# Kernel optimization log

Hardware: AMD Instinct MI355X
Metric: run time of the kernel (lower is better)

The kernel has to match this reference:

```python
import jax, jax.numpy as jnp
import numpy as np
import math

EPS = 1e-6  # PCEN eps


def _logit(p):
    return math.log(p / (1.0 - p))


def _pcen(mel, log_s, log_alpha, log_delta, log_r, dmin, dmax):
    """PCEN: per-channel energy normalization. mel: (B, M, T); params: (M,)."""
    s = jnp.clip(jax.nn.sigmoid(log_s), 0.05, 0.3)            # (M,)
    alpha = jnp.clip(jax.nn.sigmoid(log_alpha), 0.9, 0.999)   # (M,)
    delta = jnp.clip(jnp.exp(log_delta), dmin, dmax)          # (M,)
    r = jnp.clip(jax.nn.sigmoid(log_r), 0.05, 0.25)           # (M,)

    # IIR smoother over time: smoother_0 = mel[..., 0];
    # for t in 0..T-1: smoother = (1-s)*smoother + s*mel_t  (t=0 included -> smoothed_0 = mel_0)
    mel_t = jnp.transpose(mel, (2, 0, 1))  # (T, B, M)

    def step(sm, x):
        sm = (1.0 - s) * sm + s * x
        return sm, sm

    _, smoothed_t = jax.lax.scan(step, mel_t[0], mel_t)
    smoothed = jnp.transpose(smoothed_t, (1, 2, 0))  # (B, M, T)

    gain = (EPS + smoothed) ** (-alpha[None, :, None])
    d = delta[None, :, None]
    rr = r[None, :, None]
    return (mel * gain + d) ** rr - d ** rr


def setup_inputs() -> dict:
    key = jax.random.key(0)
    B, M, T = 64, 80, 4000
    mel = jax.random.uniform(key, (B, M, T), dtype=jnp.float32)
    f = jnp.full
    return {
        "mel": mel,
        # non-stationary expert PCEN (s=0.025, alpha=0.99, delta=2.0, r=0.5)
        "log_s_ns": f((M,), _logit(0.025), jnp.float32),
        "log_alpha_ns": f((M,), _logit(0.99), jnp.float32),
        "log_delta_ns": f((M,), math.log(2.0), jnp.float32),
        "log_r_ns": f((M,), _logit(0.5), jnp.float32),
        # stationary expert PCEN (s=0.15, alpha=0.99, delta=0.01, r=0.1)
        "log_s_st": f((M,), _logit(0.15), jnp.float32),
        "log_alpha_st": f((M,), _logit(0.99), jnp.float32),
        "log_delta_st": f((M,), math.log(0.01), jnp.float32),
        "log_r_st": f((M,), _logit(0.1), jnp.float32),
        "gate_temp": jnp.asarray(5.0, jnp.float32),
    }


def reference(mel, log_s_ns, log_alpha_ns, log_delta_ns, log_r_ns,
              log_s_st, log_alpha_st, log_delta_st, log_r_st, gate_temp):
    out_ns = _pcen(mel, log_s_ns, log_alpha_ns, log_delta_ns, log_r_ns, 0.5, 5.0)
    out_st = _pcen(mel, log_s_st, log_alpha_st, log_delta_st, log_r_st, 0.001, 0.1)

    # routing signal: spectral flatness + spectral tilt (0 learnable params)
    log_mel = jnp.log(mel + 1e-8)
    geo = jnp.exp(jnp.mean(log_mel, axis=1, keepdims=True))          # (B,1,T)
    arith = jnp.mean(mel, axis=1, keepdims=True) + 1e-8
    sf = jnp.clip(geo / arith, 0.0, 1.0)

    M = mel.shape[1]
    low = jnp.mean(mel[:, : M // 3, :], axis=1, keepdims=True)
    high = jnp.mean(mel[:, 2 * M // 3 :, :], axis=1, keepdims=True)
    tilt = jnp.clip(low / (low + high + 1e-8), 0.0, 1.0)

    sf_adj = sf + (1.0 - sf) * jax.nn.relu(tilt - 0.6)
    gate = jax.nn.sigmoid(gate_temp * (sf_adj - 0.5))
    return gate * out_st + (1.0 - gate) * out_ns
```

## Files before the change

kernel.cpp:

```cpp
#include <hip/hip_runtime.h>
#include <math.h>

static constexpr int kM = 80;
static constexpr int kT = 4000;
static constexpr int kB = 64;
static constexpr int kLow = kM / 3;
static constexpr int kHighStart = 2 * kM / 3;
static constexpr int kHighCount = kM - kHighStart;
static constexpr int kTrunc = 12;
#define EPSF 1e-6f
#define LOG2E 1.4426950408889634f

typedef float vfloat4 __attribute__((ext_vector_type(4)));
typedef float vfloat2 __attribute__((ext_vector_type(2)));

__device__ __forceinline__ float hw_exp2(float x) { return __builtin_amdgcn_exp2f(x); }
__device__ __forceinline__ float hw_log2(float x) { return __builtin_amdgcn_logf(x); }

__device__ __forceinline__ float fast_sigmoid(float x) {
    return __builtin_amdgcn_rcpf(1.0f + hw_exp2(-x * LOG2E));
}

__global__ __launch_bounds__(256) void gate_kernel(
    const float* __restrict__ mel,
    const float* __restrict__ gate_temp,
    float* __restrict__ gate)
{
    const int tid = threadIdx.x;
    const int c   = tid & 127;
    const int h   = tid >> 7;
    const int b   = blockIdx.y;
    const int col = blockIdx.x * 128 + c;
    const bool valid = (col < kT / 2);

    const float* base = mel + (size_t)b * kM * kT + (size_t)col * 2;

    vfloat2 slog = {0.f,0.f}, ssum = {0.f,0.f}, sband = {0.f,0.f};
    if (valid) {
        if (h == 0) {
            #pragma unroll 10
            for (int m = 0; m < 40; ++m) {
                const vfloat2 v = *reinterpret_cast<const vfloat2*>(base + (size_t)m * kT);
                vfloat2 lg;
                lg.x = hw_log2(v.x + 1e-8f);
                lg.y = hw_log2(v.y + 1e-8f);
                slog += lg;
                ssum += v;
                if (m < kLow) sband += v;
            }
        } else {
            #pragma unroll 10
            for (int m = 40; m < 80; ++m) {
                const vfloat2 v = *reinterpret_cast<const vfloat2*>(base + (size_t)m * kT);
                vfloat2 lg;
                lg.x = hw_log2(v.x + 1e-8f);
                lg.y = hw_log2(v.y + 1e-8f);
                slog += lg;
                ssum += v;
                if (m >= kHighStart) sband += v;
            }
        }
    }

    __shared__ vfloat2 p1[3][128];
    if (h == 1) {
        p1[0][c] = slog; p1[1][c] = ssum; p1[2][c] = sband;
    }
    __syncthreads();

    if (h == 0 && valid) {
        const vfloat2 tlog  = slog + p1[0][c];
        const vfloat2 tsum  = ssum + p1[1][c];
        const vfloat2 thigh = p1[2][c];
        const vfloat2 tlow  = sband;

        const float gt = gate_temp[0];
        vfloat2 o;
        #pragma unroll
        for (int q = 0; q < 2; ++q) {
            const float sl = (q == 0) ? tlog.x  : tlog.y;
            const float ss = (q == 0) ? tsum.x  : tsum.y;
            const float lo = (q == 0) ? tlow.x  : tlow.y;
            const float hi = (q == 0) ? thigh.x : thigh.y;
            const float geo   = hw_exp2(sl * (1.0f / kM));
            const float arith = ss * (1.0f / kM) + 1e-8f;
            float sf = geo * __builtin_amdgcn_rcpf(arith);
            sf = fminf(fmaxf(sf, 0.0f), 1.0f);
            const float low  = lo * (1.0f / kLow);
            const float high = hi * (1.0f / kHighCount);
            float tilt = low * __builtin_amdgcn_rcpf(low + high + 1e-8f);
            tilt = fminf(fmaxf(tilt, 0.0f), 1.0f);
            const float sfa = sf + (1.0f - sf) * fmaxf(tilt - 0.6f, 0.0f);
            const float g = fast_sigmoid(gt * (sfa - 0.5f));
            if (q == 0) o.x = g; else o.y = g;
        }
        *reinterpret_cast<vfloat2*>(gate + (size_t)b * kT + (size_t)col * 2) = o;
    }
}

__global__ __launch_bounds__(256) void pcen_kernel(
    const float* __restrict__ mel,
    const float* __restrict__ ls_ns, const float* __restrict__ la_ns,
    const float* __restrict__ ld_ns, const float* __restrict__ lr_ns,
    const float* __restrict__ ls_st, const float* __restrict__ la_st,
    const float* __restrict__ ld_st, const float* __restrict__ lr_st,
    const float* __restrict__ gate,
    float* __restrict__ out)
{
    const int m = blockIdx.x;
    const int b = blockIdx.y;

    const float s_ns     = fminf(fmaxf(fast_sigmoid(ls_ns[m]), 0.05f), 0.3f);
    const float alpha_ns = fminf(fmaxf(fast_sigmoid(la_ns[m]), 0.9f), 0.999f);
    const float delta_ns = fminf(fmaxf(hw_exp2(ld_ns[m] * LOG2E), 0.5f), 5.0f);
    const float r_ns     = fminf(fmaxf(fast_sigmoid(lr_ns[m]), 0.05f), 0.25f);
    const float s_st     = fminf(fmaxf(fast_sigmoid(ls_st[m]), 0.05f), 0.3f);
    const float alpha_st = fminf(fmaxf(fast_sigmoid(la_st[m]), 0.9f), 0.999f);
    const float delta_st = fminf(fmaxf(hw_exp2(ld_st[m] * LOG2E), 0.001f), 0.1f);
    const float r_st     = fminf(fmaxf(fast_sigmoid(lr_st[m]), 0.05f), 0.25f);
    const float dr_ns = hw_exp2(r_ns * hw_log2(delta_ns));
    const float dr_st = hw_exp2(r_st * hw_log2(delta_st));

    const vfloat2 a2 = {1.0f - s_ns, 1.0f - s_st};
    const vfloat2 s2 = {s_ns, s_st};
    const vfloat2 d2 = {delta_ns, delta_st};
    const float man = -alpha_ns, mas = -alpha_st;

    const size_t rowoff = ((size_t)b * kM + m) * kT;
    const float* row = mel + rowoff;

    const int i  = threadIdx.x;
    const int t0 = i * 16;
    const bool valid = (t0 < kT);

    float x[16];
    float gv[16];
    if (valid) {
        const float4* p = reinterpret_cast<const float4*>(row + t0);
        #pragma unroll
        for (int q = 0; q < 4; ++q) {
            const float4 v = p[q];
            x[4*q+0] = v.x; x[4*q+1] = v.y; x[4*q+2] = v.z; x[4*q+3] = v.w;
        }
        const float4* gp = reinterpret_cast<const float4*>(gate + (size_t)b * kT + t0);
        #pragma unroll
        for (int q = 0; q < 4; ++q) {
            const float4 v = gp[q];
            gv[4*q+0] = v.x; gv[4*q+1] = v.y; gv[4*q+2] = v.z; gv[4*q+3] = v.w;
        }
    } else {
        #pragma unroll
        for (int k = 0; k < 16; ++k) { x[k] = 0.0f; gv[k] = 0.0f; }
    }

    __shared__ float sv0;
    if (i == 0) sv0 = x[0];

    vfloat2 Bv = {0.0f, 0.0f};
    #pragma unroll
    for (int k = 0; k < 16; ++k) {
        Bv = a2 * Bv + s2 * x[k];
    }
    const vfloat2 p2  = a2 * a2;
    const vfloat2 p4  = p2 * p2;
    const vfloat2 p8  = p4 * p4;
    const vfloat2 A2  = p8 * p8;

    __shared__ vfloat2 Btab[256];
    Btab[i] = Bv;
    __syncthreads();

    vfloat2 sm = {0.0f, 0.0f};
    vfloat2 pw = {1.0f, 1.0f};
    #pragma unroll
    for (int k = 0; k < kTrunc; ++k) {
        const vfloat2 Bk = Btab[(i - 1 - k) & 255];
        if (k < i) {
            sm = pw * Bk + sm;
            pw = pw * A2;
        }
    }
    if (i <= kTrunc) {
        const float x0 = sv0;
        const vfloat2 x02 = {x0, x0};
        sm = pw * x02 + sm;
    }

    if (valid) {
        float4* op = reinterpret_cast<float4*>(out + rowoff + t0);
        #pragma unroll
        for (int h = 0; h < 2; ++h) {
            vfloat2 smv[8];
            #pragma unroll
            for (int j = 0; j < 8; ++j) {
                sm = a2 * sm + s2 * x[8*h + j];
                smv[j] = sm;
            }
            float res[8];
            #pragma unroll
            for (int j = 0; j < 8; ++j) {
                const int k = 8*h + j;
                const float xv = x[k];
                vfloat2 g2;
                g2.x = hw_exp2(man * hw_log2(smv[j].x + EPSF));
                g2.y = hw_exp2(mas * hw_log2(smv[j].y + EPSF));
                const vfloat2 u2 = g2 * xv + d2;
                const float on = hw_exp2(r_ns * hw_log2(u2.x)) - dr_ns;
                const float os = hw_exp2(r_st * hw_log2(u2.y)) - dr_st;
                res[j] = fmaf(gv[k], os - on, on);
            }
            #pragma unroll
            for (int q = 0; q < 2; ++q) {
                float4 v;
                v.x = res[4*q+0]; v.y = res[4*q+1];
                v.z = res[4*q+2]; v.w = res[4*q+3];
                op[2*h + q] = v;
            }
        }
    }
}

extern "C" void kernel_launch(void* const* d_in, const int* in_sizes, int n_in,
                              void* d_out, int out_size, void* d_ws, size_t ws_size,
                              hipStream_t stream)
{
    const float* mel       = (const float*)d_in[0];
    const float* ls_ns     = (const float*)d_in[1];
    const float* la_ns     = (const float*)d_in[2];
    const float* ld_ns     = (const float*)d_in[3];
    const float* lr_ns     = (const float*)d_in[4];
    const float* ls_st     = (const float*)d_in[5];
    const float* la_st     = (const float*)d_in[6];
    const float* ld_st     = (const float*)d_in[7];
    const float* lr_st     = (const float*)d_in[8];
    const float* gate_temp = (const float*)d_in[9];
    float* out  = (float*)d_out;
    float* gate = (float*)d_ws;

    dim3 gA((kT / 2 + 127) / 128, kB);
    gate_kernel<<<gA, 256, 0, stream>>>(mel, gate_temp, gate);

    dim3 gB(kM, kB);
    pcen_kernel<<<gB, 256, 0, stream>>>(mel, ls_ns, la_ns, ld_ns, lr_ns,
                                        ls_st, la_st, ld_st, lr_st, gate, out);
}
```

Baseline: 182.4 us.

## Process four rows per PCEN block with double-buffered loads; split gate reduction four ways

The PCEN kernel now gives each block four consecutive (b,m) rows and uses two register buffers, so the next row's mel load is issued before the current row is computed. This hides global load latency within a block and cuts the block count by four. The gate kernel splits the 80-channel reduction across four 64-thread groups of 20 channels each instead of two groups of 40, which doubles its grid and shortens each thread's serial load chain. The costs are more register pressure from two 16-float buffers, extra barriers per row, and fewer blocks for the PCEN kernel.

```diff
diff --git a/kernel.cpp b/kernel.cpp
--- a/kernel.cpp
+++ b/kernel.cpp
@@ -8,6 +8,7 @@
 static constexpr int kHighStart = 2 * kM / 3;
 static constexpr int kHighCount = kM - kHighStart;
 static constexpr int kTrunc = 12;
+static constexpr int kRowsPerBlock = 4;
 #define EPSF 1e-6f
 #define LOG2E 1.4426950408889634f
 
@@ -27,61 +28,53 @@
     float* __restrict__ gate)
 {
     const int tid = threadIdx.x;
-    const int c   = tid & 127;
-    const int h   = tid >> 7;
+    const int c   = tid & 63;
+    const int q   = tid >> 6;
     const int b   = blockIdx.y;
-    const int col = blockIdx.x * 128 + c;
+    const int col = blockIdx.x * 64 + c;
     const bool valid = (col < kT / 2);
 
     const float* base = mel + (size_t)b * kM * kT + (size_t)col * 2;
-
-    vfloat2 slog = {0.f,0.f}, ssum = {0.f,0.f}, sband = {0.f,0.f};
+    const int m0 = q * 20;
+
+    vfloat2 slog = {0.f,0.f}, ssum = {0.f,0.f};
+    vfloat2 slow = {0.f,0.f}, shigh = {0.f,0.f};
     if (valid) {
-        if (h == 0) {
-            #pragma unroll 10
-            for (int m = 0; m < 40; ++m) {
-                const vfloat2 v = *reinterpret_cast<const vfloat2*>(base + (size_t)m * kT);
-                vfloat2 lg;
-                lg.x = hw_log2(v.x + 1e-8f);
-                lg.y = hw_log2(v.y + 1e-8f);
-                slog += lg;
-                ssum += v;
-                if (m < kLow) sband += v;
-            }
-        } else {
-            #pragma unroll 10
-            for (int m = 40; m < 80; ++m) {
-                const vfloat2 v = *reinterpret_cast<const vfloat2*>(base + (size_t)m * kT);
-                vfloat2 lg;
-                lg.x = hw_log2(v.x + 1e-8f);
-                lg.y = hw_log2(v.y + 1e-8f);
-                slog += lg;
-                ssum += v;
-                if (m >= kHighStart) sband += v;
-            }
+        #pragma unroll
+        for (int j = 0; j < 20; ++j) {
+            const int m = m0 + j;
+            const vfloat2 v = *reinterpret_cast<const vfloat2*>(base + (size_t)m * kT);
+            vfloat2 lg;
+            lg.x = hw_log2(v.x + 1e-8f);
+            lg.y = hw_log2(v.y + 1e-8f);
+            slog += lg;
+            ssum += v;
+            if (m < kLow)        slow  += v;
+            if (m >= kHighStart) shigh += v;
         }
     }
 
-    __shared__ vfloat2 p1[3][128];
-    if (h == 1) {
-        p1[0][c] = slog; p1[1][c] = ssum; p1[2][c] = sband;
-    }
+    __shared__ vfloat2 p[4][4][64];
+    p[q][0][c] = slog;
+    p[q][1][c] = ssum;
+    p[q][2][c] = slow;
+    p[q][3][c] = shigh;
     __syncthreads();
 
-    if (h == 0 && valid) {
-        const vfloat2 tlog  = slog + p1[0][c];
-        const vfloat2 tsum  = ssum + p1[1][c];
-        const vfloat2 thigh = p1[2][c];
-        const vfloat2 tlow  = sband;
+    if (q == 0 && valid) {
+        const vfloat2 tlog  = p[0][0][c] + p[1][0][c] + p[2][0][c] + p[3][0][c];
+        const vfloat2 tsum  = p[0][1][c] + p[1][1][c] + p[2][1][c] + p[3][1][c];
+        const vfloat2 tlow  = p[0][2][c] + p[1][2][c] + p[2][2][c] + p[3][2][c];
+        const vfloat2 thigh = p[0][3][c] + p[1][3][c] + p[2][3][c] + p[3][3][c];
 
         const float gt = gate_temp[0];
         vfloat2 o;
         #pragma unroll
-        for (int q = 0; q < 2; ++q) {
-            const float sl = (q == 0) ? tlog.x  : tlog.y;
-            const float ss = (q == 0) ? tsum.x  : tsum.y;
-            const float lo = (q == 0) ? tlow.x  : tlow.y;
-            const float hi = (q == 0) ? thigh.x : thigh.y;
+        for (int w = 0; w < 2; ++w) {
+            const float sl = (w == 0) ? tlog.x  : tlog.y;
+            const float ss = (w == 0) ? tsum.x  : tsum.y;
+            const float lo = (w == 0) ? tlow.x  : tlow.y;
+            const float hi = (w == 0) ? thigh.x : thigh.y;
             const float geo   = hw_exp2(sl * (1.0f / kM));
             const float arith = ss * (1.0f / kM) + 1e-8f;
             float sf = geo * __builtin_amdgcn_rcpf(arith);
@@ -92,7 +85,7 @@
             tilt = fminf(fmaxf(tilt, 0.0f), 1.0f);
             const float sfa = sf + (1.0f - sf) * fmaxf(tilt - 0.6f, 0.0f);
             const float g = fast_sigmoid(gt * (sfa - 0.5f));
-            if (q == 0) o.x = g; else o.y = g;
+            if (w == 0) o.x = g; else o.y = g;
         }
         *reinterpret_cast<vfloat2*>(gate + (size_t)b * kT + (size_t)col * 2) = o;
     }
@@ -107,117 +100,136 @@
     const float* __restrict__ gate,
     float* __restrict__ out)
 {
-    const int m = blockIdx.x;
-    const int b = blockIdx.y;
-
-    const float s_ns     = fminf(fmaxf(fast_sigmoid(ls_ns[m]), 0.05f), 0.3f);
-    const float alpha_ns = fminf(fmaxf(fast_sigmoid(la_ns[m]), 0.9f), 0.999f);
-    const float delta_ns = fminf(fmaxf(hw_exp2(ld_ns[m] * LOG2E), 0.5f), 5.0f);
-    const float r_ns     = fminf(fmaxf(fast_sigmoid(lr_ns[m]), 0.05f), 0.25f);
-    const float s_st     = fminf(fmaxf(fast_sigmoid(ls_st[m]), 0.05f), 0.3f);
-    const float alpha_st = fminf(fmaxf(fast_sigmoid(la_st[m]), 0.9f), 0.999f);
-    const float delta_st = fminf(fmaxf(hw_exp2(ld_st[m] * LOG2E), 0.001f), 0.1f);
-    const float r_st     = fminf(fmaxf(fast_sigmoid(lr_st[m]), 0.05f), 0.25f);
-    const float dr_ns = hw_exp2(r_ns * hw_log2(delta_ns));
-    const float dr_st = hw_exp2(r_st * hw_log2(delta_st));
-
-    const vfloat2 a2 = {1.0f - s_ns, 1.0f - s_st};
-    const vfloat2 s2 = {s_ns, s_st};
-    const vfloat2 d2 = {delta_ns, delta_st};
-    const float man = -alpha_ns, mas = -alpha_st;
-
-    const size_t rowoff = ((size_t)b * kM + m) * kT;
-    const float* row = mel + rowoff;
-
     const int i  = threadIdx.x;
     const int t0 = i * 16;
     const bool valid = (t0 < kT);
 
-    float x[16];
-    float gv[16];
-    if (valid) {
-        const float4* p = reinterpret_cast<const float4*>(row + t0);
-        #pragma unroll
-        for (int q = 0; q < 4; ++q) {
-            const float4 v = p[q];
-            x[4*q+0] = v.x; x[4*q+1] = v.y; x[4*q+2] = v.z; x[4*q+3] = v.w;
-        }
-        const float4* gp = reinterpret_cast<const float4*>(gate + (size_t)b * kT + t0);
-        #pragma unroll
-        for (int q = 0; q < 4; ++q) {
-            const float4 v = gp[q];
-            gv[4*q+0] = v.x; gv[4*q+1] = v.y; gv[4*q+2] = v.z; gv[4*q+3] = v.w;
-        }
-    } else {
-        #pragma unroll
-        for (int k = 0; k < 16; ++k) { x[k] = 0.0f; gv[k] = 0.0f; }
-    }
-
+    __shared__ vfloat2 Btab[256];
     __shared__ float sv0;
-    if (i == 0) sv0 = x[0];
-
-    vfloat2 Bv = {0.0f, 0.0f};
-    #pragma unroll
-    for (int k = 0; k < 16; ++k) {
-        Bv = a2 * Bv + s2 * x[k];
-    }
-    const vfloat2 p2  = a2 * a2;
-    const vfloat2 p4  = p2 * p2;
-    const vfloat2 p8  = p4 * p4;
-    const vfloat2 A2  = p8 * p8;
-
-    __shared__ vfloat2 Btab[256];
-    Btab[i] = Bv;
-    __syncthreads();
-
-    vfloat2 sm = {0.0f, 0.0f};
-    vfloat2 pw = {1.0f, 1.0f};
-    #pragma unroll
-    for (int k = 0; k < kTrunc; ++k) {
-        const vfloat2 Bk = Btab[(i - 1 - k) & 255];
-        if (k < i) {
-            sm = pw * Bk + sm;
-            pw = pw * A2;
-        }
-    }
-    if (i <= kTrunc) {
-        const float x0 = sv0;
-        const vfloat2 x02 = {x0, x0};
-        sm = pw * x02 + sm;
-    }
-
-    if (valid) {
-        float4* op = reinterpret_cast<float4*>(out + rowoff + t0);
-        #pragma unroll
-        for (int h = 0; h < 2; ++h) {
-            vfloat2 smv[8];
-            #pragma unroll
-            for (int j = 0; j < 8; ++j) {
-                sm = a2 * sm + s2 * x[8*h + j];
-                smv[j] = sm;
-            }
-            float res[8];
-            #pragma unroll
-            for (int j = 0; j < 8; ++j) {
-                const int k = 8*h + j;
-                const float xv = x[k];
-                vfloat2 g2;
-                g2.x = hw_exp2(man * hw_log2(smv[j].x + EPSF));
-                g2.y = hw_exp2(mas * hw_log2(smv[j].y + EPSF));
-                const vfloat2 u2 = g2 * xv + d2;
-                const float on = hw_exp2(r_ns * hw_log2(u2.x)) - dr_ns;
-                const float os = hw_exp2(r_st * hw_log2(u2.y)) - dr_st;
-                res[j] = fmaf(gv[k], os - on, on);
-            }
-            #pragma unroll
-            for (int q = 0; q < 2; ++q) {
-                float4 v;
-                v.x = res[4*q+0]; v.y = res[4*q+1];
-                v.z = res[4*q+2]; v.w = res[4*q+3];
-                op[2*h + q] = v;
-            }
-        }
-    }
+
+    float xA[16], xB[16];
+    const int r0 = blockIdx.x * kRowsPerBlock;
+
+    auto load_x = [&](float* x, int row) {
+        if (valid) {
+            const float4* p = reinterpret_cast<const float4*>(mel + (size_t)row * kT + t0);
+            #pragma unroll
+            for (int u = 0; u < 4; ++u) {
+                const float4 v = p[u];
+                x[4*u+0] = v.x; x[4*u+1] = v.y; x[4*u+2] = v.z; x[4*u+3] = v.w;
+            }
+        } else {
+            #pragma unroll
+            for (int k = 0; k < 16; ++k) x[k] = 0.0f;
+        }
+    };
+
+    auto process = [&](const float* x, int row) {
+        const int b = row / kM;
+        const int m = row - b * kM;
+
+        const float s_ns     = fminf(fmaxf(fast_sigmoid(ls_ns[m]), 0.05f), 0.3f);
+        const float alpha_ns = fminf(fmaxf(fast_sigmoid(la_ns[m]), 0.9f), 0.999f);
+        const float delta_ns = fminf(fmaxf(hw_exp2(ld_ns[m] * LOG2E), 0.5f), 5.0f);
+        const float r_ns     = fminf(fmaxf(fast_sigmoid(lr_ns[m]), 0.05f), 0.25f);
+        const float s_st     = fminf(fmaxf(fast_sigmoid(ls_st[m]), 0.05f), 0.3f);
+        const float alpha_st = fminf(fmaxf(fast_sigmoid(la_st[m]), 0.9f), 0.999f);
+        const float delta_st = fminf(fmaxf(hw_exp2(ld_st[m] * LOG2E), 0.001f), 0.1f);
+        const float r_st     = fminf(fmaxf(fast_sigmoid(lr_st[m]), 0.05f), 0.25f);
+        const float dr_ns = hw_exp2(r_ns * hw_log2(delta_ns));
+        const float dr_st = hw_exp2(r_st * hw_log2(delta_st));
+
+        const vfloat2 a2 = {1.0f - s_ns, 1.0f - s_st};
+        const vfloat2 s2 = {s_ns, s_st};
+        const vfloat2 d2 = {delta_ns, delta_st};
+        const float man = -alpha_ns, mas = -alpha_st;
+
+        float gv[16];
+        if (valid) {
+            const float4* gp = reinterpret_cast<const float4*>(gate + (size_t)b * kT + t0);
+            #pragma unroll
+            for (int u = 0; u < 4; ++u) {
+                const float4 v = gp[u];
+                gv[4*u+0] = v.x; gv[4*u+1] = v.y; gv[4*u+2] = v.z; gv[4*u+3] = v.w;
+            }
+        } else {
+            #pragma unroll
+            for (int k = 0; k < 16; ++k) gv[k] = 0.0f;
+        }
+
+        vfloat2 Bv = {0.0f, 0.0f};
+        #pragma unroll
+        for (int k = 0; k < 16; ++k) {
+            Bv = a2 * Bv + s2 * x[k];
+        }
+        const vfloat2 p2 = a2 * a2;
+        const vfloat2 p4 = p2 * p2;
+        const vfloat2 p8 = p4 * p4;
+        const vfloat2 A2 = p8 * p8;
+
+        __syncthreads();
+        Btab[i] = Bv;
+        if (i == 0) sv0 = x[0];
+        __syncthreads();
+
+        vfloat2 sm = {0.0f, 0.0f};
+        vfloat2 pw = {1.0f, 1.0f};
+        #pragma unroll
+        for (int k = 0; k < kTrunc; ++k) {
+            const vfloat2 Bk = Btab[(i - 1 - k) & 255];
+            if (k < i) {
+                sm = pw * Bk + sm;
+                pw = pw * A2;
+            }
+        }
+        if (i <= kTrunc) {
+            const float x0 = sv0;
+            const vfloat2 x02 = {x0, x0};
+            sm = pw * x02 + sm;
+        }
+
+        if (valid) {
+            float4* op = reinterpret_cast<float4*>(out + (size_t)row * kT + t0);
+            #pragma unroll
+            for (int h = 0; h < 2; ++h) {
+                vfloat2 smv[8];
+                #pragma unroll
+                for (int j = 0; j < 8; ++j) {
+                    sm = a2 * sm + s2 * x[8*h + j];
+                    smv[j] = sm;
+                }
+                float res[8];
+                #pragma unroll
+                for (int j = 0; j < 8; ++j) {
+                    const int k = 8*h + j;
+                    const float xv = x[k];
+                    vfloat2 g2;
+                    g2.x = hw_exp2(man * hw_log2(smv[j].x + EPSF));
+                    g2.y = hw_exp2(mas * hw_log2(smv[j].y + EPSF));
+                    const vfloat2 u2 = g2 * xv + d2;
+                    const float on = hw_exp2(r_ns * hw_log2(u2.x)) - dr_ns;
+                    const float os = hw_exp2(r_st * hw_log2(u2.y)) - dr_st;
+                    res[j] = fmaf(gv[k], os - on, on);
+                }
+                #pragma unroll
+                for (int u = 0; u < 2; ++u) {
+                    float4 v;
+                    v.x = res[4*u+0]; v.y = res[4*u+1];
+                    v.z = res[4*u+2]; v.w = res[4*u+3];
+                    op[2*h + u] = v;
+                }
+            }
+        }
+    };
+
+    load_x(xA, r0 + 0);
+    load_x(xB, r0 + 1);
+    process(xA, r0 + 0);
+    load_x(xA, r0 + 2);
+    process(xB, r0 + 1);
+    load_x(xB, r0 + 3);
+    process(xA, r0 + 2);
+    process(xB, r0 + 3);
 }
 
 extern "C" void kernel_launch(void* const* d_in, const int* in_sizes, int n_in,
@@ -237,10 +249,10 @@
     float* out  = (float*)d_out;
     float* gate = (float*)d_ws;
 
-    dim3 gA((kT / 2 + 127) / 128, kB);
+    dim3 gA((kT / 2 + 63) / 64, kB);
     gate_kernel<<<gA, 256, 0, stream>>>(mel, gate_temp, gate);
 
-    dim3 gB(kM, kB);
-    pcen_kernel<<<gB, 256, 0, stream>>>(mel, ls_ns, la_ns, ld_ns, lr_ns,
-                                        ls_st, la_st, ld_st, lr_st, gate, out);
-}
+    const int nblk = kB * kM / kRowsPerBlock;
+    pcen_kernel<<<dim3(nblk), 256, 0, stream>>>(mel, ls_ns, la_ns, ld_ns, lr_ns,
+                                                ls_st, la_st, ld_st, lr_st, gate, out);
+}
```

After: 189.7 us. +4.0%, slower.
